# Kernel optimization log

Hardware: AMD Instinct MI355X
Metric: run time of the kernel (lower is better)

## Reference

```python
import jax, jax.numpy as jnp
import numpy as np

B, T, D = 4, 512, 512
NB, NH, PF, K = 2, 8, 2, 4
INNER = PF * D          # 1024
DH = INNER // NH        # 128
NC = 1000
EPS = 1e-5


def _ln(x, s, b):
    mu = x.mean(-1, keepdims=True)
    var = x.var(-1, keepdims=True)
    return (x - mu) / jnp.sqrt(var + EPS) * s + b


def _causal_conv(x, k, b):
    # x: [B,T,C], depthwise kernel k: [C,K]
    kk = k.shape[-1]
    xp = jnp.pad(x, ((0, 0), (kk - 1, 0), (0, 0)))
    t = x.shape[1]
    y = sum(xp[:, j:j + t, :] * k[:, j] for j in range(kk))
    return y + b


def _mlstm_scan(q, k, v, ip, fp):
    # q,k,v: [B,T,NH,DH]; ip,fp: [B,T,NH]
    b, t, nh, dh = q.shape
    C0 = jnp.zeros((b, nh, dh, dh), q.dtype)
    n0 = jnp.zeros((b, nh, dh), q.dtype)
    m0 = jnp.zeros((b, nh), q.dtype)

    def step(carry, xs):
        C, n, m = carry
        qt, kt, vt, ipt, fpt = xs
        fl = jax.nn.log_sigmoid(fpt)
        m_new = jnp.maximum(fl + m, ipt)
        i = jnp.exp(ipt - m_new)
        f = jnp.exp(fl + m - m_new)
        C = f[..., None, None] * C + i[..., None, None] * (vt[..., :, None] * kt[..., None, :])
        n = f[..., None] * n + i[..., None] * kt
        denom = jnp.maximum(jnp.abs(jnp.einsum('bhd,bhd->bh', n, qt)), 1.0)
        h = jnp.einsum('bhij,bhj->bhi', C, qt) / denom[..., None]
        return (C, n, m_new), h

    tm = lambda a: jnp.swapaxes(a, 0, 1)  # time-major
    _, h = jax.lax.scan(step, (C0, n0, m0), (tm(q), tm(k), tm(v), tm(ip), tm(fp)))
    return jnp.swapaxes(h, 0, 1)  # [B,T,NH,DH]


def _block(x, ln_s, ln_b, w_up, b_up, conv_k, conv_b, w_q, w_k, w_v,
           w_ig, b_ig, w_fg, b_fg, hn_s, w_down, b_down):
    b, t, d = x.shape
    xn = _ln(x, ln_s, ln_b)
    up = xn @ w_up + b_up                       # [B,T,2*INNER]
    xu, z = up[..., :INNER], up[..., INNER:]
    xc = jax.nn.silu(_causal_conv(xu, conv_k, conv_b))
    q = (xc @ w_q).reshape(b, t, NH, DH)
    k = (xc @ w_k).reshape(b, t, NH, DH) * (DH ** -0.5)
    v = (xu @ w_v).reshape(b, t, NH, DH)
    ip = xc @ w_ig + b_ig                       # [B,T,NH]
    fp = xc @ w_fg + b_fg
    h = _mlstm_scan(q, k, v, ip, fp)            # [B,T,NH,DH]
    mu = h.mean(-1, keepdims=True)
    var = h.var(-1, keepdims=True)
    h = (h - mu) / jnp.sqrt(var + EPS) * hn_s   # per-head norm, hn_s: [NH,DH]
    h = h.reshape(b, t, INNER) * jax.nn.silu(z)
    return x + h @ w_down + b_down


def setup_inputs() -> dict:
    key = jax.random.key(0)
    ks = jax.random.split(key, 24)
    g = lambda i, sh, sc: jax.random.normal(ks[i], sh, jnp.float32) * sc
    inp = {
        'x': g(0, (B, T, D), 1.0),
        'cls_token': g(1, (1, 1, D), 0.02),
        'ln_s': jnp.ones((NB, D)), 'ln_b': jnp.zeros((NB, D)),
        'w_up': g(2, (NB, D, 2 * INNER), D ** -0.5), 'b_up': jnp.zeros((NB, 2 * INNER)),
        'conv_k': g(3, (NB, INNER, K), 0.3), 'conv_b': jnp.zeros((NB, INNER)),
        'w_q': g(4, (NB, INNER, INNER), INNER ** -0.5),
        'w_k': g(5, (NB, INNER, INNER), INNER ** -0.5),
        'w_v': g(6, (NB, INNER, INNER), INNER ** -0.5),
        'w_ig': g(7, (NB, INNER, NH), INNER ** -0.5), 'b_ig': jnp.zeros((NB, NH)),
        'w_fg': g(8, (NB, INNER, NH), INNER ** -0.5),
        'b_fg': jnp.full((NB, NH), 3.0),
        'hn_s': jnp.ones((NB, NH, DH)),
        'w_down': g(9, (NB, INNER, D), INNER ** -0.5), 'b_down': jnp.zeros((NB, D)),
        'fc_ln_s': jnp.ones((D,)), 'fc_ln_b': jnp.zeros((D,)),
        'fc_w': g(10, (D, NC), D ** -0.5), 'fc_b': jnp.zeros((NC,)),
    }
    return inp


def reference(x, cls_token, ln_s, ln_b, w_up, b_up, conv_k, conv_b, w_q, w_k, w_v,
              w_ig, b_ig, w_fg, b_fg, hn_s, w_down, b_down,
              fc_ln_s, fc_ln_b, fc_w, fc_b):
    b = x.shape[0]
    # append class token at the last position ('last')
    h = jnp.concatenate([x, jnp.broadcast_to(cls_token, (b, 1, x.shape[-1]))], axis=1)
    for i in range(NB):
        h = _block(h, ln_s[i], ln_b[i], w_up[i], b_up[i], conv_k[i], conv_b[i],
                   w_q[i], w_k[i], w_v[i], w_ig[i], b_ig[i], w_fg[i], b_fg[i],
                   hn_s[i], w_down[i], b_down[i])
    cls = h[:, -1, :]
    y = jax.nn.relu(_ln(cls, fc_ln_s, fc_ln_b)) @ fc_w + fc_b
    return y
```

## Files before the change

kernel.cpp:

```cpp
#include <hip/hip_runtime.h>

#define EPSV 1e-5f
constexpr int Bsz = 4, T0 = 512, Dm = 512, TT = 513, NHh = 8, KK = 4;
constexpr int IN = 1024, DHd = 128, NCc = 1000;
constexpr int ROWS = Bsz * TT;
constexpr int MPAD = 2176;
constexpr int NCH = 9;

constexpr size_t WT_UP = 0;
constexpr size_t WT_Q  = WT_UP + 2048 * 512;
constexpr size_t WT_K  = WT_Q + 1024 * 1024;
constexpr size_t WT_V  = WT_K + 1024 * 1024;
constexpr size_t WT_DN = WT_V + 1024 * 1024;
constexpr size_t WT_STRIDE = WT_DN + 512 * 1024;

typedef __attribute__((ext_vector_type(8))) short bf16x8;
typedef __attribute__((ext_vector_type(4))) float f32x4;
typedef __attribute__((ext_vector_type(4))) unsigned short ushort4v;
typedef __attribute__((ext_vector_type(8))) unsigned short ushort8v;
typedef unsigned short u16;

__device__ __forceinline__ float siluf(float x) { return x / (1.f + __expf(-x)); }
__device__ __forceinline__ u16 f2bf(float f) {
    unsigned int u = __float_as_uint(f);
    u = (u + 0x7FFFu + ((u >> 16) & 1u)) >> 16;
    return (u16)u;
}
__device__ __forceinline__ float bfu(u16 u) {
    return __uint_as_float(((unsigned int)u) << 16);
}
__device__ __forceinline__ void gload16(const u16* g, u16* l) {
    __builtin_amdgcn_global_load_lds(
        (const __attribute__((address_space(1))) void*)g,
        (__attribute__((address_space(3))) void*)l, 16, 0, 0);
}

__global__ __launch_bounds__(256) void concat_kernel(const float* __restrict__ x,
                                                     const float* __restrict__ cls,
                                                     float* __restrict__ h) {
    int idx = blockIdx.x * 256 + threadIdx.x;
    if (idx >= Bsz * TT * Dm) return;
    int d = idx & (Dm - 1);
    int bt = idx >> 9;
    int t = bt % TT, b = bt / TT;
    h[idx] = (t < T0) ? x[((size_t)(b * T0 + t)) * Dm + d] : cls[d];
}

__global__ __launch_bounds__(256) void ln_kernel(const float* __restrict__ in,
                                                 const float* __restrict__ s,
                                                 const float* __restrict__ bb,
                                                 u16* __restrict__ out16) {
    int row = blockIdx.x, tid = threadIdx.x;
    const float* r = in + (size_t)row * Dm;
    __shared__ float s1[4], s2[4];
    float x0 = r[tid], x1 = r[tid + 256];
    float sum = x0 + x1, sq = x0 * x0 + x1 * x1;
#pragma unroll
    for (int o = 32; o > 0; o >>= 1) { sum += __shfl_xor(sum, o); sq += __shfl_xor(sq, o); }
    if ((tid & 63) == 0) { s1[tid >> 6] = sum; s2[tid >> 6] = sq; }
    __syncthreads();
    sum = s1[0] + s1[1] + s1[2] + s1[3];
    sq  = s2[0] + s2[1] + s2[2] + s2[3];
    float mu = sum / Dm, var = sq / Dm - mu * mu, inv = rsqrtf(var + EPSV);
    out16[(size_t)row * Dm + tid]       = f2bf((x0 - mu) * inv * s[tid] + bb[tid]);
    out16[(size_t)row * Dm + tid + 256] = f2bf((x1 - mu) * inv * s[tid + 256] + bb[tid + 256]);
}

__global__ __launch_bounds__(256) void w_transpose_kernel(const float* __restrict__ wup,
        const float* __restrict__ wq, const float* __restrict__ wk,
        const float* __restrict__ wv, const float* __restrict__ wdn,
        u16* __restrict__ wt) {
    int y = blockIdx.y;
    int blk = y / 5, sel = y - blk * 5;
    int Kd, N; const float* src; size_t doff;
    if (sel == 0)      { Kd = 512;  N = 2048; src = wup + (size_t)blk * 512 * 2048; doff = WT_UP; }
    else if (sel == 1) { Kd = 1024; N = 1024; src = wq  + (size_t)blk * 1024 * 1024; doff = WT_Q; }
    else if (sel == 2) { Kd = 1024; N = 1024; src = wk  + (size_t)blk * 1024 * 1024; doff = WT_K; }
    else if (sel == 3) { Kd = 1024; N = 1024; src = wv  + (size_t)blk * 1024 * 1024; doff = WT_V; }
    else               { Kd = 1024; N = 512;  src = wdn + (size_t)blk * 1024 * 512;  doff = WT_DN; }
    u16* dst = wt + (size_t)blk * WT_STRIDE + doff;
    int ntx = N >> 5;
    int ntiles = ntx * (Kd >> 5);
    int ti = blockIdx.x;
    if (ti >= ntiles) return;
    int tk = ti / ntx, tn = ti - tk * ntx;
    __shared__ u16 s[32][33];
    int tx = threadIdx.x & 31, ty = threadIdx.x >> 5;
#pragma unroll
    for (int i = 0; i < 4; i++) {
        int k = tk * 32 + ty + i * 8;
        s[ty + i * 8][tx] = f2bf(src[(size_t)k * N + tn * 32 + tx]);
    }
    __syncthreads();
#pragma unroll
    for (int i = 0; i < 4; i++) {
        int n = tn * 32 + ty + i * 8;
        dst[(size_t)n * Kd + tk * 32 + tx] = s[tx][ty + i * 8];
    }
}

template<int BM, int BN>
__device__ __forceinline__ void gemm_tile_body(const u16* __restrict__ A, int lda,
                                               const u16* __restrict__ Wt, int Kd,
                                               const float* __restrict__ bias,
                                               const float* __restrict__ resid, int ldr,
                                               float* __restrict__ Cout, int ldc,
                                               int M, float scale, int m0, int n0,
                                               u16 (*As)[BM][40], u16 (*Bs)[BN][40]) {
    constexpr int MT = BM / 32;
    constexpr int NT = BN / 32;
    constexpr int ANV = BM / 64;
    constexpr int BNV = BN / 64;
    int tid = threadIdx.x;
    int wave = tid >> 6, lane = tid & 63;
    int wm = (wave >> 1) * (BM / 2), wn = (wave & 1) * (BN / 2);
    int lrow = lane & 15, lquad = lane >> 4;

    f32x4 acc[MT][NT];
#pragma unroll
    for (int i = 0; i < MT; i++)
#pragma unroll
        for (int j = 0; j < NT; j++)
#pragma unroll
            for (int r = 0; r < 4; r++) acc[i][j][r] = 0.f;

    int am, ak, bn, bk;
    if (BM == 128) { am = tid >> 1; ak = (tid & 1) * 16; }
    else           { am = tid >> 2; ak = (tid & 3) * 8; }
    if (BN == 128) { bn = tid & 127; bk = (tid >> 7) * 16; }
    else           { bn = tid & 63;  bk = (tid >> 6) * 8; }
    int gm = m0 + am;
    const u16* arow = A + (size_t)(gm < M ? gm : 0) * lda + ak;
    bool avalid = gm < M;
    const u16* wrow = Wt + (size_t)(n0 + bn) * Kd + bk;

    ushort8v areg[ANV];
    ushort8v breg[BNV];

    auto load_tile = [&](int k0) {
        if (avalid) {
#pragma unroll
            for (int i = 0; i < ANV; i++) areg[i] = *(const ushort8v*)(arow + k0 + i * 8);
        } else {
#pragma unroll
            for (int i = 0; i < ANV; i++) areg[i] = (ushort8v){0,0,0,0,0,0,0,0};
        }
#pragma unroll
        for (int i = 0; i < BNV; i++) breg[i] = *(const ushort8v*)(wrow + k0 + i * 8);
    };
    auto store_tile = [&](int buf) {
#pragma unroll
        for (int i = 0; i < ANV; i++)
            *(ushort8v*)&As[buf][am][ak + i * 8] = areg[i];
#pragma unroll
        for (int i = 0; i < BNV; i++)
            *(ushort8v*)&Bs[buf][bn][bk + i * 8] = breg[i];
    };

    load_tile(0);
    store_tile(0);
    __syncthreads();

    int nk = Kd >> 5;
#pragma unroll 1
    for (int it = 0; it < nk; it++) {
        int cur = it & 1;
        bool more = (it + 1 < nk);
        if (more) load_tile((it + 1) << 5);
        bf16x8 afr[MT], bfr[NT];
#pragma unroll
        for (int mt = 0; mt < MT; mt++)
            afr[mt] = *(const bf16x8*)&As[cur][wm + mt * 16 + lrow][lquad * 8];
#pragma unroll
        for (int nt = 0; nt < NT; nt++)
            bfr[nt] = *(const bf16x8*)&Bs[cur][wn + nt * 16 + lrow][lquad * 8];
#pragma unroll
        for (int mt = 0; mt < MT; mt++)
#pragma unroll
            for (int nt = 0; nt < NT; nt++)
                acc[mt][nt] = __builtin_amdgcn_mfma_f32_16x16x32_bf16(
                    afr[mt], bfr[nt], acc[mt][nt], 0, 0, 0);
        if (more) store_tile(cur ^ 1);
        __syncthreads();
    }

#pragma unroll
    for (int mt = 0; mt < MT; mt++) {
#pragma unroll
        for (int r = 0; r < 4; r++) {
            int gmr = m0 + wm + mt * 16 + lquad * 4 + r;
            if (gmr >= M) continue;
#pragma unroll
            for (int nt = 0; nt < NT; nt++) {
                int gn = n0 + wn + nt * 16 + lrow;
                float v = acc[mt][nt][r] * scale;
                if (bias) v += bias[gn];
                if (resid) v += resid[(size_t)gmr * ldr + gn];
                Cout[(size_t)gmr * ldc + gn] = v;
            }
        }
    }
}

template<int BM, int BN>
__global__ __launch_bounds__(256, 2) void gemm_mfma_kernel(const u16* __restrict__ A, int lda,
                                                           const u16* __restrict__ Wt, int Kd,
                                                           const float* __restrict__ bias,
                                                           const float* __restrict__ resid, int ldr,
                                                           float* __restrict__ Cout, int ldc,
                                                           int M, float scale) {
    __shared__ __align__(16) u16 As[2][BM][40];
    __shared__ __align__(16) u16 Bs[2][BN][40];
    gemm_tile_body<BM, BN>(A, lda, Wt, Kd, bias, resid, ldr, Cout, ldc, M, scale,
                           blockIdx.y * BM, blockIdx.x * BN, As, Bs);
}

__device__ __forceinline__ void gemm128_body(const u16* __restrict__ A, int lda,
                                             const u16* __restrict__ Wt, int Kd,
                                             const float* __restrict__ bias,
                                             float* __restrict__ Cout, int ldc,
                                             int M, float scale, int m0, int n0,
                                             u16* As, u16* Bs) {
    int tid = threadIdx.x;
    int wave = tid >> 6, lane = tid & 63;
    int lrow = lane & 15, lquad = lane >> 4;
    int wm = (wave >> 1) * 64, wn = (wave & 1) * 64;

    const u16* ag0 = A + (size_t)(m0 + wave * 16 + (lane >> 2)) * lda + (lane & 3) * 8;
    const u16* ag1 = ag0 + (size_t)64 * lda;
    const u16* bg0 = Wt + (size_t)(n0 + wave * 16 + (lane >> 2)) * Kd + (lane & 3) * 8;
    const u16* bg1 = bg0 + (size_t)64 * Kd;
    u16* la0 = As + wave * 512;
    u16* la1 = As + 2048 + wave * 512;
    u16* lb0 = Bs + wave * 512;
    u16* lb1 = Bs + 2048 + wave * 512;

    f32x4 acc[4][4];
#pragma unroll
    for (int i = 0; i < 4; i++)
#pragma unroll
        for (int j = 0; j < 4; j++)
#pragma unroll
            for (int r = 0; r < 4; r++) acc[i][j][r] = 0.f;

    int nk = Kd >> 5;
#pragma unroll 1
    for (int it = 0; it < nk; it++) {
        int k0 = it << 5;
        gload16(ag0 + k0, la0);
        gload16(ag1 + k0, la1);
        gload16(bg0 + k0, lb0);
        gload16(bg1 + k0, lb1);
        __syncthreads();
        bf16x8 afr[4], bfr[4];
#pragma unroll
        for (int mt = 0; mt < 4; mt++)
            afr[mt] = *(const bf16x8*)&As[(wm + mt * 16 + lrow) * 32 + lquad * 8];
#pragma unroll
        for (int nt = 0; nt < 4; nt++)
            bfr[nt] = *(const bf16x8*)&Bs[(wn + nt * 16 + lrow) * 32 + lquad * 8];
#pragma unroll
        for (int mt = 0; mt < 4; mt++)
#pragma unroll
            for (int nt = 0; nt < 4; nt++)
                acc[mt][nt] = __builtin_amdgcn_mfma_f32_16x16x32_bf16(
                    afr[mt], bfr[nt], acc[mt][nt], 0, 0, 0);
        __syncthreads();
    }

#pragma unroll
    for (int mt = 0; mt < 4; mt++) {
#pragma unroll
        for (int r = 0; r < 4; r++) {
            int gmr = m0 + wm + mt * 16 + lquad * 4 + r;
            if (gmr >= M) continue;
#pragma unroll
            for (int nt = 0; nt < 4; nt++) {
                int gn = n0 + wn + nt * 16 + lrow;
                float v = acc[mt][nt][r] * scale;
                if (bias) v += bias[gn];
                Cout[(size_t)gmr * ldc + gn] = v;
            }
        }
    }
}

__global__ __launch_bounds__(256, 2) void up_gl_kernel(const u16* __restrict__ A,
        const u16* __restrict__ Wt, const float* __restrict__ bias, float* __restrict__ C) {
    __shared__ __align__(16) u16 As[128 * 32];
    __shared__ __align__(16) u16 Bs[128 * 32];
    gemm128_body(A, Dm, Wt, Dm, bias, C, 2 * IN, ROWS, 1.f,
                 blockIdx.y * 128, blockIdx.x * 128, As, Bs);
}

__global__ __launch_bounds__(256, 2) void qkv_gl_kernel(const u16* __restrict__ xc16,
                                                        const u16* __restrict__ xu16,
                                                        const u16* __restrict__ wtblk,
                                                        float* __restrict__ fq,
                                                        float* __restrict__ fk,
                                                        float* __restrict__ fv,
                                                        float kscale) {
    __shared__ __align__(16) u16 As[128 * 32];
    __shared__ __align__(16) u16 Bs[128 * 32];
    int sel = blockIdx.x >> 3, nx = blockIdx.x & 7;
    const u16* A = (sel == 2) ? xu16 : xc16;
    const u16* Wt = wtblk + ((sel == 0) ? WT_Q : (sel == 1) ? WT_K : WT_V);
    float* C = (sel == 0) ? fq : (sel == 1) ? fk : fv;
    float scale = (sel == 1) ? kscale : 1.f;
    gemm128_body(A, IN, Wt, IN, nullptr, C, IN, ROWS, scale,
                 blockIdx.y * 128, nx * 128, As, Bs);
}

__global__ __launch_bounds__(256) void convgates_kernel(const float* __restrict__ up,
        const float* __restrict__ ck, const float* __restrict__ cb,
        const float* __restrict__ wt, const float* __restrict__ big,
        const float* __restrict__ bfg,
        u16* __restrict__ xc16, u16* __restrict__ xu16,
        float* __restrict__ ip, float* __restrict__ fp) {
    int row = blockIdx.x, tid = threadIdx.x;
    int b = row / TT, t = row - b * TT;
    __shared__ float sx[IN];
    int c0 = tid * 4;
    float4 cur = *(const float4*)(up + (size_t)row * (2 * IN) + c0);
    float a0 = cb[c0 + 0] + cur.x * ck[(c0 + 0) * KK + 3];
    float a1 = cb[c0 + 1] + cur.y * ck[(c0 + 1) * KK + 3];
    float a2 = cb[c0 + 2] + cur.z * ck[(c0 + 2) * KK + 3];
    float a3 = cb[c0 + 3] + cur.w * ck[(c0 + 3) * KK + 3];
#pragma unroll
    for (int j = 0; j < KK - 1; j++) {
        int tt2 = t - (KK - 1) + j;
        if (tt2 >= 0) {
            float4 pv = *(const float4*)(up + ((size_t)(b * TT + tt2)) * (2 * IN) + c0);
            a0 += pv.x * ck[(c0 + 0) * KK + j];
            a1 += pv.y * ck[(c0 + 1) * KK + j];
            a2 += pv.z * ck[(c0 + 2) * KK + j];
            a3 += pv.w * ck[(c0 + 3) * KK + j];
        }
    }
    float s0 = siluf(a0), s1v = siluf(a1), s2v = siluf(a2), s3v = siluf(a3);
    *(float4*)&sx[c0] = make_float4(s0, s1v, s2v, s3v);
    ushort4v xc4 = {f2bf(s0), f2bf(s1v), f2bf(s2v), f2bf(s3v)};
    *(ushort4v*)&xc16[(size_t)row * IN + c0] = xc4;
    ushort4v xu4 = {f2bf(cur.x), f2bf(cur.y), f2bf(cur.z), f2bf(cur.w)};
    *(ushort4v*)&xu16[(size_t)row * IN + c0] = xu4;
    __syncthreads();

    int g = tid >> 4, l = tid & 15;
    const float* wrow = wt + g * IN;
    float acc = 0.f;
#pragma unroll
    for (int j = 0; j < 16; j++) {
        int k = j * 64 + l * 4;
        float4 w4 = *(const float4*)(wrow + k);
        float4 x4 = *(const float4*)&sx[k];
        acc += w4.x * x4.x + w4.y * x4.y + w4.z * x4.z + w4.w * x4.w;
    }
#pragma unroll
    for (int o = 8; o > 0; o >>= 1) acc += __shfl_down(acc, o, 16);
    if (l == 0) {
        if (g < 8) ip[(size_t)row * NHh + g] = acc + big[g];
        else       fp[(size_t)row * NHh + (g - 8)] = acc + bfg[g - 8];
    }
}

__global__ __launch_bounds__(64) void gate_scan_kernel(const float* __restrict__ ip,
        const float* __restrict__ fp, float* __restrict__ gG, float* __restrict__ gM,
        float* __restrict__ gMb, float* __restrict__ gDec) {
    constexpr int PER = 9;
    int chain = blockIdx.x;
    int b = chain >> 3, h = chain & 7;
    int lane = threadIdx.x;
    int tbase = lane * PER;
    float lcs[PER];
    float gi[PER];
    float csum = 0.f;
#pragma unroll
    for (int i = 0; i < PER; i++) {
        int t = tbase + i;
        float fpv = 0.f, ipv = 0.f;
        if (t < TT) {
            size_t gidx = (size_t)(b * TT + t) * NHh + h;
            fpv = fp[gidx]; ipv = ip[gidx];
        }
        float flv = (fpv >= 0.f) ? -log1pf(__expf(-fpv)) : (fpv - log1pf(__expf(fpv)));
        if (t >= TT) flv = 0.f;
        csum += flv;
        lcs[i] = csum;
        gi[i] = ipv;
    }
    float ps = csum;
#pragma unroll
    for (int o = 1; o < 64; o <<= 1) {
        float v = __shfl_up(ps, o);
        if (lane >= o) ps += v;
    }
    float Fexcl = ps - csum;
    float G[PER];
    float cmax = -1e30f;
#pragma unroll
    for (int i = 0; i < PER; i++) {
        int t = tbase + i;
        G[i] = (t < TT) ? (gi[i] - (Fexcl + lcs[i])) : -1e30f;
        cmax = fmaxf(cmax, G[i]);
        lcs[i] = cmax;
    }
    float pm = cmax;
#pragma unroll
    for (int o = 1; o < 64; o <<= 1) {
        float v = __shfl_up(pm, o);
        if (lane >= o) pm = fmaxf(pm, v);
    }
    float Me = __shfl_up(pm, 1);
    if (lane == 0) Me = -1e30f;
    __shared__ float sMb[NCH];
#pragma unroll
    for (int i = 0; i < PER; i++) {
        int t = tbase + i;
        if (t < TT) {
            float Mt = fmaxf(0.f, fmaxf(Me, lcs[i]));
            gG[chain * TT + t] = G[i];
            gM[chain * TT + t] = Mt;
            if (((t & 63) == 63) || t == TT - 1) sMb[t >> 6] = Mt;
        }
    }
    __syncthreads();
    if (lane < NCH) {
        float Mb = sMb[lane];
        float Mbp = (lane == 0) ? 0.f : sMb[lane - 1];
        gMb[chain * NCH + lane] = Mb;
        gDec[chain * NCH + lane] = __expf(Mbp - Mb);
    }
}

__global__ __launch_bounds__(256, 2) void chunk_state_kernel(const float* __restrict__ kk,
        const float* __restrict__ vv, const float* __restrict__ gG,
        const float* __restrict__ gMb, float* __restrict__ P, float* __restrict__ nP) {
    int c = blockIdx.x, chain = blockIdx.y;
    int b = chain >> 3, h = chain & 7;
    int t0 = c * 64;
    int nvalid = min(64, TT - t0);
    __shared__ __align__(16) u16 sWv[128][72];
    __shared__ __align__(16) u16 sKt[128][72];
    __shared__ float sw[64];
    int tid = threadIdx.x;
    if (tid < 64) {
        float Mb = gMb[chain * NCH + c];
        sw[tid] = (tid < nvalid) ? __expf(gG[chain * TT + t0 + tid] - Mb) : 0.f;
    }
    __syncthreads();

    {
        int j = tid >> 2, d0 = (tid & 3) * 32;
        bool val = j < nvalid;
        float wj = sw[j];
        size_t gb = ((size_t)(b * TT + t0 + j)) * IN + h * DHd + d0;
#pragma unroll
        for (int i = 0; i < 8; i++) {
            float4 k4 = val ? *(const float4*)(kk + gb + i * 4) : make_float4(0.f, 0.f, 0.f, 0.f);
            float4 v4 = val ? *(const float4*)(vv + gb + i * 4) : make_float4(0.f, 0.f, 0.f, 0.f);
            int dd = d0 + i * 4;
            int jc = j ^ (((dd >> 5) & 3) << 4);
            sKt[dd + 0][jc] = f2bf(k4.x);
            sKt[dd + 1][jc] = f2bf(k4.y);
            sKt[dd + 2][jc] = f2bf(k4.z);
            sKt[dd + 3][jc] = f2bf(k4.w);
            sWv[dd + 0][jc] = f2bf(v4.x * wj);
            sWv[dd + 1][jc] = f2bf(v4.y * wj);
            sWv[dd + 2][jc] = f2bf(v4.z * wj);
            sWv[dd + 3][jc] = f2bf(v4.w * wj);
        }
    }
    __syncthreads();

    int wave = tid >> 6, lane = tid & 63;
    int lrow = lane & 15, lquad = lane >> 4;
    int wm = (wave >> 1) * 64, wn = (wave & 1) * 64;
    f32x4 acc[4][4];
#pragma unroll
    for (int mt = 0; mt < 4; mt++)
#pragma unroll
        for (int nt = 0; nt < 4; nt++)
#pragma unroll
            for (int r = 0; r < 4; r++) acc[mt][nt][r] = 0.f;

#pragma unroll
    for (int ks = 0; ks < 2; ks++) {
        bf16x8 af[4], bfr[4];
#pragma unroll
        for (int mt = 0; mt < 4; mt++) {
            int r = wm + mt * 16 + lrow;
            int g = (ks * 4 + lquad) ^ (((r >> 5) & 3) << 1);
            af[mt] = *(const bf16x8*)&sWv[r][g * 8];
        }
#pragma unroll
        for (int nt = 0; nt < 4; nt++) {
            int r = wn + nt * 16 + lrow;
            int g = (ks * 4 + lquad) ^ (((r >> 5) & 3) << 1);
            bfr[nt] = *(const bf16x8*)&sKt[r][g * 8];
        }
#pragma unroll
        for (int mt = 0; mt < 4; mt++)
#pragma unroll
            for (int nt = 0; nt < 4; nt++)
                acc[mt][nt] = __builtin_amdgcn_mfma_f32_16x16x32_bf16(
                    af[mt], bfr[nt], acc[mt][nt], 0, 0, 0);
    }

    float* Pbase = P + (((size_t)(c * 32 + chain)) << 14);
#pragma unroll
    for (int mt = 0; mt < 4; mt++)
#pragma unroll
        for (int r = 0; r < 4; r++) {
            int e = wm + mt * 16 + lquad * 4 + r;
#pragma unroll
            for (int nt = 0; nt < 4; nt++) {
                int d = wn + nt * 16 + lrow;
                Pbase[(size_t)e * 128 + d] = acc[mt][nt][r];
            }
        }

    {
        int d = tid >> 1, jh = (tid & 1) * 32;
        int swz = ((d >> 5) & 3) << 4;
        float an = 0.f;
#pragma unroll
        for (int j = 0; j < 32; j++) {
            int jj = jh + j;
            an += sw[jj] * bfu(sKt[d][jj ^ swz]);
        }
        an += __shfl_xor(an, 1);
        if ((tid & 1) == 0) nP[(size_t)(c * 32 + chain) * 128 + d] = an;
    }
}

__global__ __launch_bounds__(256) void chunk_combine_kernel(const float* __restrict__ P,
        u16* __restrict__ CB, float* __restrict__ nP, const float* __restrict__ gDec) {
    int chain = blockIdx.x >> 6;
    int seg = blockIdx.x & 63;
    int idx = seg * 256 + threadIdx.x;
    float run = 0.f;
    for (int c = 0; c < NCH; c++) {
        size_t a = (((size_t)(c * 32 + chain)) << 14) + idx;
        float tmp = P[a];
        CB[a] = f2bf(run);
        run = run * gDec[chain * NCH + c] + tmp;
    }
    if (seg == 0 && threadIdx.x < 128) {
        int d = threadIdx.x;
        float rn = 0.f;
        for (int c = 0; c < NCH; c++) {
            size_t a = (size_t)(c * 32 + chain) * 128 + d;
            float tmp = nP[a];
            nP[a] = rn;
            rn = rn * gDec[chain * NCH + c] + tmp;
        }
    }
}

__global__ __launch_bounds__(512, 2) void chunk_out_kernel(const float* __restrict__ qq,
        const float* __restrict__ kk, const float* __restrict__ vv,
        const float* __restrict__ gG, const float* __restrict__ gM,
        const float* __restrict__ gMb, const u16* __restrict__ CB,
        const float* __restrict__ nP, const float* __restrict__ hn,
        const float* __restrict__ up, u16* __restrict__ out16) {
    int c = blockIdx.x, chain = blockIdx.y;
    int b = chain >> 3, h = chain & 7;
    int t0 = c * 64;
    int nvalid = min(64, TT - t0);
    __shared__ __align__(16) u16 smem[30720];
    __shared__ float sG[64], sM[64], sWr[64], sInv[64], sNb[128], sRS[2][64];
    u16* sQ  = smem;
    u16* sCB = smem + 8704;
    u16* sK  = smem + 8704;
    u16* sVt = smem;
    u16* sD  = smem + 26112;
    float* hv = (float*)smem;
    int tid = threadIdx.x;
    int wave = tid >> 6, lane = tid & 63;
    int lrow = lane & 15, lquad = lane >> 4;
    int mq = wave >> 1, nh = wave & 1;

    float Mbprev = (c > 0) ? gMb[chain * NCH + c - 1] : 0.f;
    if (tid < 64) {
        bool val = tid < nvalid;
        sG[tid] = val ? gG[chain * TT + t0 + tid] : -1e30f;
        float Mv = val ? gM[chain * TT + t0 + tid] : 1e30f;
        sM[tid] = Mv;
        sWr[tid] = val ? __expf(Mbprev - Mv) : 0.f;
    }
    if (tid >= 128 && tid < 256) sNb[tid - 128] = nP[(size_t)(c * 32 + chain) * 128 + (tid - 128)];

    {
        int lr = tid >> 3, c0 = (tid & 7) * 16;
        bool val = lr < nvalid;
        size_t gb = ((size_t)(b * TT + t0 + lr)) * IN + h * DHd + c0;
#pragma unroll
        for (int i = 0; i < 4; i++) {
            float4 q4 = val ? *(const float4*)(qq + gb + i * 4) : make_float4(0.f,0.f,0.f,0.f);
            ushort4v tq = {f2bf(q4.x), f2bf(q4.y), f2bf(q4.z), f2bf(q4.w)};
            *(ushort4v*)&sQ[lr * 136 + c0 + i * 4] = tq;
        }
    }
    {
        const u16* CBbase = CB + (((size_t)(c * 32 + chain)) << 14);
        int e = tid >> 2, d0 = (tid & 3) * 32;
#pragma unroll
        for (int i = 0; i < 4; i++)
            *(ushort8v*)&sCB[e * 136 + d0 + i * 8] =
                *(const ushort8v*)(CBbase + (size_t)e * 128 + d0 + i * 8);
    }
    __syncthreads();

    f32x4 acc[4];
#pragma unroll
    for (int tt = 0; tt < 4; tt++)
#pragma unroll
        for (int r = 0; r < 4; r++) acc[tt][r] = 0.f;
#pragma unroll 1
    for (int ks = 0; ks < 4; ks++) {
        bf16x8 af = *(const bf16x8*)&sQ[(mq * 16 + lrow) * 136 + ks * 32 + lquad * 8];
#pragma unroll
        for (int tt = 0; tt < 4; tt++) {
            bf16x8 bf = *(const bf16x8*)&sCB[(nh * 64 + tt * 16 + lrow) * 136 + ks * 32 + lquad * 8];
            acc[tt] = __builtin_amdgcn_mfma_f32_16x16x32_bf16(af, bf, acc[tt], 0, 0, 0);
        }
    }
#pragma unroll
    for (int tt = 0; tt < 4; tt++)
#pragma unroll
        for (int r = 0; r < 4; r++) acc[tt][r] *= sWr[mq * 16 + lquad * 4 + r];
    __syncthreads();

    {
        int lr = tid >> 3, c0 = (tid & 7) * 16;
        bool val = lr < nvalid;
        size_t gb = ((size_t)(b * TT + t0 + lr)) * IN + h * DHd + c0;
#pragma unroll
        for (int i = 0; i < 4; i++) {
            float4 k4 = val ? *(const float4*)(kk + gb + i * 4) : make_float4(0.f,0.f,0.f,0.f);
            ushort4v tk = {f2bf(k4.x), f2bf(k4.y), f2bf(k4.z), f2bf(k4.w)};
            *(ushort4v*)&sK[lr * 136 + c0 + i * 4] = tk;
        }
    }
    __syncthreads();

    {
        f32x4 accS[2];
#pragma unroll
        for (int tt = 0; tt < 2; tt++)
#pragma unroll
            for (int r = 0; r < 4; r++) accS[tt][r] = 0.f;
#pragma unroll 1
        for (int ks = 0; ks < 4; ks++) {
            bf16x8 af = *(const bf16x8*)&sQ[(mq * 16 + lrow) * 136 + ks * 32 + lquad * 8];
#pragma unroll
            for (int tt = 0; tt < 2; tt++) {
                bf16x8 bf = *(const bf16x8*)&sK[((nh * 2 + tt) * 16 + lrow) * 136 + ks * 32 + lquad * 8];
                accS[tt] = __builtin_amdgcn_mfma_f32_16x16x32_bf16(af, bf, accS[tt], 0, 0, 0);
            }
        }
        float rsum[4] = {0.f, 0.f, 0.f, 0.f};
#pragma unroll
        for (int tt = 0; tt < 2; tt++) {
            int j = (nh * 2 + tt) * 16 + lrow;
            float Gj = sG[j];
#pragma unroll
            for (int r = 0; r < 4; r++) {
                int t = mq * 16 + lquad * 4 + r;
                float w = (j <= t) ? __expf(Gj - sM[t]) : 0.f;
                float wD = accS[tt][r] * w;
                rsum[r] += wD;
                sD[t * 72 + j] = f2bf(wD);
            }
        }
#pragma unroll
        for (int r = 0; r < 4; r++) {
#pragma unroll
            for (int msk = 1; msk < 16; msk <<= 1) rsum[r] += __shfl_xor(rsum[r], msk);
        }
        if (lrow == 0) {
#pragma unroll
            for (int r = 0; r < 4; r++) sRS[nh][mq * 16 + lquad * 4 + r] = rsum[r];
        }
    }
    __syncthreads();

    if (tid < 64) {
        float qn = 0.f;
#pragma unroll 1
        for (int d4 = 0; d4 < 32; d4++) {
            ushort4v q4 = *(const ushort4v*)&sQ[tid * 136 + d4 * 4];
            float4 nb = *(const float4*)&sNb[d4 * 4];
            qn += bfu(q4.x) * nb.x + bfu(q4.y) * nb.y + bfu(q4.z) * nb.z + bfu(q4.w) * nb.w;
        }
        float den = sRS[0][tid] + sRS[1][tid] + sWr[tid] * qn;
        sInv[tid] = 1.f / fmaxf(fabsf(den), 1.f);
    }
    __syncthreads();

    {
        int e = tid & 127, tg = (tid >> 7) * 16;
#pragma unroll 1
        for (int i = 0; i < 16; i++) {
            int t = tg + i;
            float v = (t < nvalid) ? vv[((size_t)(b * TT + t0 + t)) * IN + h * DHd + e] : 0.f;
            sVt[e * 72 + t] = f2bf(v);
        }
    }
    __syncthreads();

#pragma unroll 1
    for (int ks = 0; ks < 2; ks++) {
        bf16x8 af = *(const bf16x8*)&sD[(mq * 16 + lrow) * 72 + ks * 32 + lquad * 8];
#pragma unroll
        for (int tt = 0; tt < 4; tt++) {
            bf16x8 bf = *(const bf16x8*)&sVt[(nh * 64 + tt * 16 + lrow) * 72 + ks * 32 + lquad * 8];
            acc[tt] = __builtin_amdgcn_mfma_f32_16x16x32_bf16(af, bf, acc[tt], 0, 0, 0);
        }
    }

    __syncthreads();
#pragma unroll
    for (int tt = 0; tt < 4; tt++) {
#pragma unroll
        for (int r = 0; r < 4; r++) {
            int t = mq * 16 + lquad * 4 + r;
            int e = nh * 64 + tt * 16 + lrow;
            hv[t * 132 + e] = acc[tt][r] * sInv[t];
        }
    }
    __syncthreads();
    {
        int t = tid >> 3, s = tid & 7;
        float vals[16];
        float sum = 0.f, sq = 0.f;
#pragma unroll
        for (int i = 0; i < 16; i++) {
            float v = hv[t * 132 + s * 16 + i];
            vals[i] = v; sum += v; sq += v * v;
        }
#pragma unroll
        for (int m = 1; m < 8; m <<= 1) { sum += __shfl_xor(sum, m); sq += __shfl_xor(sq, m); }
        float mu = sum / DHd, var = sq / DHd - mu * mu, inv2 = rsqrtf(var + EPSV);
        if (t < nvalid) {
            size_t bt = (size_t)(b * TT + t0 + t);
            const float* zp = up + bt * (2 * IN) + IN + h * DHd + s * 16;
            u16* op = out16 + bt * IN + h * DHd + s * 16;
#pragma unroll
            for (int i = 0; i < 16; i++) {
                float hnv = hn[h * DHd + s * 16 + i];
                op[i] = f2bf((vals[i] - mu) * inv2 * hnv * siluf(zp[i]));
            }
        }
    }
}

__global__ __launch_bounds__(256) void fc_kernel(const float* __restrict__ hbuf,
                                                 const float* __restrict__ fcls,
                                                 const float* __restrict__ fclb,
                                                 const float* __restrict__ fw,
                                                 const float* __restrict__ fb,
                                                 float* __restrict__ out) {
    __shared__ float svc[Bsz][Dm];
    __shared__ float sred[4][256];
    int tid = threadIdx.x;
    int j0 = blockIdx.x * 64;
    {
        int r = tid >> 6, lane = tid & 63;
        const float* hrow = hbuf + ((size_t)r * TT + TT - 1) * Dm;
        float v[8];
        float sum = 0.f, sq = 0.f;
#pragma unroll
        for (int k = 0; k < 8; k++) {
            v[k] = hrow[lane + k * 64];
            sum += v[k]; sq += v[k] * v[k];
        }
#pragma unroll
        for (int o = 32; o > 0; o >>= 1) { sum += __shfl_xor(sum, o); sq += __shfl_xor(sq, o); }
        float mu = sum / Dm, var = sq / Dm - mu * mu, inv = rsqrtf(var + EPSV);
#pragma unroll
        for (int k = 0; k < 8; k++) {
            int e = lane + k * 64;
            svc[r][e] = fmaxf((v[k] - mu) * inv * fcls[e] + fclb[e], 0.f);
        }
    }
    __syncthreads();
    int j = j0 + (tid & 63);
    int chunk = tid >> 6;
    int kbase = chunk * 128;
    float a0 = 0.f, a1 = 0.f, a2 = 0.f, a3 = 0.f;
    if (j < NCc) {
        const float* fwp = fw + (size_t)kbase * NCc + j;
#pragma unroll 4
        for (int kk = 0; kk < 128; kk++) {
            float w = fwp[(size_t)kk * NCc];
            a0 += svc[0][kbase + kk] * w;
            a1 += svc[1][kbase + kk] * w;
            a2 += svc[2][kbase + kk] * w;
            a3 += svc[3][kbase + kk] * w;
        }
    }
    int jl = tid & 63;
    sred[chunk][jl * 4 + 0] = a0;
    sred[chunk][jl * 4 + 1] = a1;
    sred[chunk][jl * 4 + 2] = a2;
    sred[chunk][jl * 4 + 3] = a3;
    __syncthreads();
    if (tid < 64) {
        int jj = j0 + tid;
        if (jj < NCc) {
            float bias = fb[jj];
#pragma unroll
            for (int b = 0; b < Bsz; b++) {
                float v = sred[0][tid * 4 + b] + sred[1][tid * 4 + b]
                        + sred[2][tid * 4 + b] + sred[3][tid * 4 + b];
                out[b * NCc + jj] = v + bias;
            }
        }
    }
}

__global__ __launch_bounds__(256) void gate_w_transpose(const float* __restrict__ wig,
                                                        const float* __restrict__ wfg,
                                                        float* __restrict__ wt) {
    int idx = blockIdx.x * 256 + threadIdx.x;
    int k = idx & 1023;
    int g = (idx >> 10) & 15;
    int blk = idx >> 14;
    const float* w = (g < 8) ? (wig + (size_t)blk * IN * NHh) : (wfg + (size_t)blk * IN * NHh);
    wt[idx] = w[k * NHh + (g & 7)];
}

extern "C" void kernel_launch(void* const* d_in, const int* in_sizes, int n_in,
                              void* d_out, int out_size, void* d_ws, size_t ws_size,
                              hipStream_t stream) {
    const float* x      = (const float*)d_in[0];
    const float* cls    = (const float*)d_in[1];
    const float* ln_s   = (const float*)d_in[2];
    const float* ln_b   = (const float*)d_in[3];
    const float* w_up   = (const float*)d_in[4];
    const float* b_up   = (const float*)d_in[5];
    const float* conv_k = (const float*)d_in[6];
    const float* conv_b = (const float*)d_in[7];
    const float* w_q    = (const float*)d_in[8];
    const float* w_k    = (const float*)d_in[9];
    const float* w_v    = (const float*)d_in[10];
    const float* w_ig   = (const float*)d_in[11];
    const float* b_ig   = (const float*)d_in[12];
    const float* w_fg   = (const float*)d_in[13];
    const float* b_fg   = (const float*)d_in[14];
    const float* hn_s   = (const float*)d_in[15];
    const float* w_down = (const float*)d_in[16];
    const float* b_down = (const float*)d_in[17];
    const float* fcls   = (const float*)d_in[18];
    const float* fclb   = (const float*)d_in[19];
    const float* fc_w   = (const float*)d_in[20];
    const float* fc_b   = (const float*)d_in[21];
    float* out = (float*)d_out;

    float* ws = (float*)d_ws;
    size_t off = 0;
    float* f_h  = ws + off; off += (size_t)ROWS * Dm;
    float* f_up = ws + off; off += (size_t)ROWS * 2 * IN;
    float* f_q  = ws + off; off += (size_t)ROWS * IN;
    float* f_k  = ws + off; off += (size_t)ROWS * IN;
    float* f_v  = ws + off; off += (size_t)ROWS * IN;
    float* f_ip = ws + off; off += (size_t)ROWS * NHh;
    float* f_fp = ws + off; off += (size_t)ROWS * NHh;
    float* g_G  = ws + off; off += 32 * TT;
    float* g_M  = ws + off; off += 32 * TT;
    float* g_Mb = ws + off; off += 32 * NCH;
    float* g_De = ws + off; off += 32 * NCH;
    float* g_P  = ws + off; off += (size_t)NCH * 32 * DHd * DHd;
    float* g_nP = ws + off; off += (size_t)NCH * 32 * DHd;
    float* g_wt = ws + off; off += 2 * 16 * IN;
    u16* g_CB  = (u16*)(ws + off); off += ((size_t)NCH * 32 * DHd * DHd + 1) / 2;
    u16* g_Wt  = (u16*)(ws + off); off += (2 * WT_STRIDE + 1) / 2;
    u16* f_xn16 = (u16*)(ws + off); off += ((size_t)MPAD * Dm) / 2;
    u16* f_xc16 = (u16*)(ws + off); off += ((size_t)MPAD * IN) / 2;
    u16* f_xu16 = (u16*)(ws + off); off += ((size_t)MPAD * IN) / 2;
    u16* f_xg16 = (u16*)(ws + off); off += ((size_t)ROWS * IN + 1) / 2;

    const float kscale = 0.08838834764831845f;
    const int MB = (ROWS + 127) / 128;
    const int MB64 = (ROWS + 63) / 64;

    concat_kernel<<<(ROWS * Dm + 255) / 256, 256, 0, stream>>>(x, cls, f_h);
    gate_w_transpose<<<(2 * 16 * IN + 255) / 256, 256, 0, stream>>>(w_ig, w_fg, g_wt);
    w_transpose_kernel<<<dim3(1024, 10), 256, 0, stream>>>(w_up, w_q, w_k, w_v, w_down, g_Wt);

    for (int blk = 0; blk < 2; blk++) {
        const float* p_ln_s = ln_s + blk * Dm;
        const float* p_ln_b = ln_b + blk * Dm;
        const float* p_bup  = b_up + (size_t)blk * 2 * IN;
        const float* p_ck   = conv_k + (size_t)blk * IN * KK;
        const float* p_cb   = conv_b + (size_t)blk * IN;
        const float* p_big  = b_ig + (size_t)blk * NHh;
        const float* p_bfg  = b_fg + (size_t)blk * NHh;
        const float* p_hns  = hn_s + (size_t)blk * NHh * DHd;
        const float* p_bd   = b_down + (size_t)blk * Dm;
        const u16*   p_wt   = g_Wt + (size_t)blk * WT_STRIDE;

        ln_kernel<<<ROWS, 256, 0, stream>>>(f_h, p_ln_s, p_ln_b, f_xn16);

        up_gl_kernel<<<dim3(2 * IN / 128, MB), 256, 0, stream>>>(
            f_xn16, p_wt + WT_UP, p_bup, f_up);

        convgates_kernel<<<ROWS, 256, 0, stream>>>(
            f_up, p_ck, p_cb, g_wt + blk * 16 * IN, p_big, p_bfg,
            f_xc16, f_xu16, f_ip, f_fp);

        qkv_gl_kernel<<<dim3(24, MB), 256, 0, stream>>>(
            f_xc16, f_xu16, p_wt, f_q, f_k, f_v, kscale);

        gate_scan_kernel<<<32, 64, 0, stream>>>(f_ip, f_fp, g_G, g_M, g_Mb, g_De);
        chunk_state_kernel<<<dim3(NCH, 32), 256, 0, stream>>>(f_k, f_v, g_G, g_Mb, g_P, g_nP);
        chunk_combine_kernel<<<32 * 64, 256, 0, stream>>>(g_P, g_CB, g_nP, g_De);
        chunk_out_kernel<<<dim3(NCH, 32), 512, 0, stream>>>(f_q, f_k, f_v, g_G, g_M, g_Mb,
                                                            g_CB, g_nP, p_hns, f_up, f_xg16);

        gemm_mfma_kernel<64, 64><<<dim3(Dm / 64, MB64), 256, 0, stream>>>(
            f_xg16, IN, p_wt + WT_DN, IN, p_bd, f_h, Dm, f_h, Dm, ROWS, 1.f);
    }

    fc_kernel<<<(NCc + 63) / 64, 256, 0, stream>>>(f_h, fcls, fclb, fc_w, fc_b, out);
}
```

Measured before the change: 435.4 us.

## Store q/k/v as bf16 and double-buffer LDS in 128-tile GEMM

```diff
diff --git a/kernel.cpp b/kernel.cpp
--- a/kernel.cpp
+++ b/kernel.cpp
@@ -1,7 +1,8 @@
 #include <hip/hip_runtime.h>
 
 #define EPSV 1e-5f
-constexpr int Bsz = 4, T0 = 512, Dm = 512, TT = 513, NHh = 8, KK = 4;
+constexpr int Bsz = 4, T0 = 512, Dm = 512, NHh = 8, KK = 4;
+constexpr int TT = 513;
 constexpr int IN = 1024, DHd = 128, NCc = 1000;
 constexpr int ROWS = Bsz * TT;
 constexpr int MPAD = 2176;
@@ -215,10 +216,11 @@
                            blockIdx.y * BM, blockIdx.x * BN, As, Bs);
 }
 
+template<bool OUT16>
 __device__ __forceinline__ void gemm128_body(const u16* __restrict__ A, int lda,
                                              const u16* __restrict__ Wt, int Kd,
                                              const float* __restrict__ bias,
-                                             float* __restrict__ Cout, int ldc,
+                                             void* __restrict__ Cout, int ldc,
                                              int M, float scale, int m0, int n0,
                                              u16* As, u16* Bs) {
     int tid = threadIdx.x;
@@ -230,10 +232,15 @@
     const u16* ag1 = ag0 + (size_t)64 * lda;
     const u16* bg0 = Wt + (size_t)(n0 + wave * 16 + (lane >> 2)) * Kd + (lane & 3) * 8;
     const u16* bg1 = bg0 + (size_t)64 * Kd;
-    u16* la0 = As + wave * 512;
-    u16* la1 = As + 2048 + wave * 512;
-    u16* lb0 = Bs + wave * 512;
-    u16* lb1 = Bs + 2048 + wave * 512;
+
+    auto stage = [&](int buf, int k0) {
+        u16* a = As + buf * 4096 + wave * 512;
+        u16* bb = Bs + buf * 4096 + wave * 512;
+        gload16(ag0 + k0, a);
+        gload16(ag1 + k0, a + 2048);
+        gload16(bg0 + k0, bb);
+        gload16(bg1 + k0, bb + 2048);
+    };
 
     f32x4 acc[4][4];
 #pragma unroll
@@ -244,21 +251,21 @@
             for (int r = 0; r < 4; r++) acc[i][j][r] = 0.f;
 
     int nk = Kd >> 5;
+    stage(0, 0);
+    __syncthreads();
 #pragma unroll 1
     for (int it = 0; it < nk; it++) {
-        int k0 = it << 5;
-        gload16(ag0 + k0, la0);
-        gload16(ag1 + k0, la1);
-        gload16(bg0 + k0, lb0);
-        gload16(bg1 + k0, lb1);
-        __syncthreads();
+        int cur = it & 1;
+        if (it + 1 < nk) stage(cur ^ 1, (it + 1) << 5);
+        const u16* Ac = As + cur * 4096;
+        const u16* Bc = Bs + cur * 4096;
         bf16x8 afr[4], bfr[4];
 #pragma unroll
         for (int mt = 0; mt < 4; mt++)
-            afr[mt] = *(const bf16x8*)&As[(wm + mt * 16 + lrow) * 32 + lquad * 8];
+            afr[mt] = *(const bf16x8*)&Ac[(wm + mt * 16 + lrow) * 32 + lquad * 8];
 #pragma unroll
         for (int nt = 0; nt < 4; nt++)
-            bfr[nt] = *(const bf16x8*)&Bs[(wn + nt * 16 + lrow) * 32 + lquad * 8];
+            bfr[nt] = *(const bf16x8*)&Bc[(wn + nt * 16 + lrow) * 32 + lquad * 8];
 #pragma unroll
         for (int mt = 0; mt < 4; mt++)
 #pragma unroll
@@ -279,7 +286,8 @@
                 int gn = n0 + wn + nt * 16 + lrow;
                 float v = acc[mt][nt][r] * scale;
                 if (bias) v += bias[gn];
-                Cout[(size_t)gmr * ldc + gn] = v;
+                if (OUT16) ((u16*)Cout)[(size_t)gmr * ldc + gn] = f2bf(v);
+                else       ((float*)Cout)[(size_t)gmr * ldc + gn] = v;
             }
         }
     }
@@ -287,28 +295,28 @@
 
 __global__ __launch_bounds__(256, 2) void up_gl_kernel(const u16* __restrict__ A,
         const u16* __restrict__ Wt, const float* __restrict__ bias, float* __restrict__ C) {
-    __shared__ __align__(16) u16 As[128 * 32];
-    __shared__ __align__(16) u16 Bs[128 * 32];
-    gemm128_body(A, Dm, Wt, Dm, bias, C, 2 * IN, ROWS, 1.f,
-                 blockIdx.y * 128, blockIdx.x * 128, As, Bs);
+    __shared__ __align__(16) u16 As[2 * 4096];
+    __shared__ __align__(16) u16 Bs[2 * 4096];
+    gemm128_body<false>(A, Dm, Wt, Dm, bias, C, 2 * IN, ROWS, 1.f,
+                        blockIdx.y * 128, blockIdx.x * 128, As, Bs);
 }
 
 __global__ __launch_bounds__(256, 2) void qkv_gl_kernel(const u16* __restrict__ xc16,
                                                         const u16* __restrict__ xu16,
                                                         const u16* __restrict__ wtblk,
-                                                        float* __restrict__ fq,
-                                                        float* __restrict__ fk,
-                                                        float* __restrict__ fv,
+                                                        u16* __restrict__ fq,
+                                                        u16* __restrict__ fk,
+                                                        u16* __restrict__ fv,
                                                         float kscale) {
-    __shared__ __align__(16) u16 As[128 * 32];
-    __shared__ __align__(16) u16 Bs[128 * 32];
+    __shared__ __align__(16) u16 As[2 * 4096];
+    __shared__ __align__(16) u16 Bs[2 * 4096];
     int sel = blockIdx.x >> 3, nx = blockIdx.x & 7;
     const u16* A = (sel == 2) ? xu16 : xc16;
     const u16* Wt = wtblk + ((sel == 0) ? WT_Q : (sel == 1) ? WT_K : WT_V);
-    float* C = (sel == 0) ? fq : (sel == 1) ? fk : fv;
+    u16* C = (sel == 0) ? fq : (sel == 1) ? fk : fv;
     float scale = (sel == 1) ? kscale : 1.f;
-    gemm128_body(A, IN, Wt, IN, nullptr, C, IN, ROWS, scale,
-                 blockIdx.y * 128, nx * 128, As, Bs);
+    gemm128_body<true>(A, IN, Wt, IN, nullptr, C, IN, ROWS, scale,
+                       blockIdx.y * 128, nx * 128, As, Bs);
 }
 
 __global__ __launch_bounds__(256) void convgates_kernel(const float* __restrict__ up,
@@ -432,8 +440,8 @@
     }
 }
 
-__global__ __launch_bounds__(256, 2) void chunk_state_kernel(const float* __restrict__ kk,
-        const float* __restrict__ vv, const float* __restrict__ gG,
+__global__ __launch_bounds__(256, 2) void chunk_state_kernel(const u16* __restrict__ kk,
+        const u16* __restrict__ vv, const float* __restrict__ gG,
         const float* __restrict__ gMb, float* __restrict__ P, float* __restrict__ nP) {
     int c = blockIdx.x, chain = blockIdx.y;
     int b = chain >> 3, h = chain & 7;
@@ -454,20 +462,18 @@
         bool val = j < nvalid;
         float wj = sw[j];
         size_t gb = ((size_t)(b * TT + t0 + j)) * IN + h * DHd + d0;
-#pragma unroll
-        for (int i = 0; i < 8; i++) {
-            float4 k4 = val ? *(const float4*)(kk + gb + i * 4) : make_float4(0.f, 0.f, 0.f, 0.f);
-            float4 v4 = val ? *(const float4*)(vv + gb + i * 4) : make_float4(0.f, 0.f, 0.f, 0.f);
-            int dd = d0 + i * 4;
-            int jc = j ^ (((dd >> 5) & 3) << 4);
-            sKt[dd + 0][jc] = f2bf(k4.x);
-            sKt[dd + 1][jc] = f2bf(k4.y);
-            sKt[dd + 2][jc] = f2bf(k4.z);
-            sKt[dd + 3][jc] = f2bf(k4.w);
-            sWv[dd + 0][jc] = f2bf(v4.x * wj);
-            sWv[dd + 1][jc] = f2bf(v4.y * wj);
-            sWv[dd + 2][jc] = f2bf(v4.z * wj);
-            sWv[dd + 3][jc] = f2bf(v4.w * wj);
+        ushort8v z8 = {0,0,0,0,0,0,0,0};
+#pragma unroll
+        for (int i = 0; i < 4; i++) {
+            ushort8v k8 = val ? *(const ushort8v*)(kk + gb + i * 8) : z8;
+            ushort8v v8 = val ? *(const ushort8v*)(vv + gb + i * 8) : z8;
+#pragma unroll
+            for (int e = 0; e < 8; e++) {
+                int dd = d0 + i * 8 + e;
+                int jc = j ^ (((dd >> 5) & 3) << 4);
+                sKt[dd][jc] = k8[e];
+                sWv[dd][jc] = f2bf(bfu(v8[e]) * wj);
+            }
         }
     }
     __syncthreads();
@@ -557,8 +563,8 @@
     }
 }
 
-__global__ __launch_bounds__(512, 2) void chunk_out_kernel(const float* __restrict__ qq,
-        const float* __restrict__ kk, const float* __restrict__ vv,
+__global__ __launch_bounds__(512, 2) void chunk_out_kernel(const u16* __restrict__ qq,
+        const u16* __restrict__ kk, const u16* __restrict__ vv,
         const float* __restrict__ gG, const float* __restrict__ gM,
         const float* __restrict__ gMb, const u16* __restrict__ CB,
         const float* __restrict__ nP, const float* __restrict__ hn,
@@ -590,16 +596,15 @@
     }
     if (tid >= 128 && tid < 256) sNb[tid - 128] = nP[(size_t)(c * 32 + chain) * 128 + (tid - 128)];
 
+    ushort8v z8 = {0,0,0,0,0,0,0,0};
     {
         int lr = tid >> 3, c0 = (tid & 7) * 16;
         bool val = lr < nvalid;
         size_t gb = ((size_t)(b * TT + t0 + lr)) * IN + h * DHd + c0;
 #pragma unroll
-        for (int i = 0; i < 4; i++) {
-            float4 q4 = val ? *(const float4*)(qq + gb + i * 4) : make_float4(0.f,0.f,0.f,0.f);
-            ushort4v tq = {f2bf(q4.x), f2bf(q4.y), f2bf(q4.z), f2bf(q4.w)};
-            *(ushort4v*)&sQ[lr * 136 + c0 + i * 4] = tq;
-        }
+        for (int i = 0; i < 2; i++)
+            *(ushort8v*)&sQ[lr * 136 + c0 + i * 8] =
+                val ? *(const ushort8v*)(qq + gb + i * 8) : z8;
     }
     {
         const u16* CBbase = CB + (((size_t)(c * 32 + chain)) << 14);
@@ -636,11 +641,9 @@
         bool val = lr < nvalid;
         size_t gb = ((size_t)(b * TT + t0 + lr)) * IN + h * DHd + c0;
 #pragma unroll
-        for (int i = 0; i < 4; i++) {
-            float4 k4 = val ? *(const float4*)(kk + gb + i * 4) : make_float4(0.f,0.f,0.f,0.f);
-            ushort4v tk = {f2bf(k4.x), f2bf(k4.y), f2bf(k4.z), f2bf(k4.w)};
-            *(ushort4v*)&sK[lr * 136 + c0 + i * 4] = tk;
-        }
+        for (int i = 0; i < 2; i++)
+            *(ushort8v*)&sK[lr * 136 + c0 + i * 8] =
+                val ? *(const ushort8v*)(kk + gb + i * 8) : z8;
     }
     __syncthreads();
 
@@ -703,8 +706,8 @@
 #pragma unroll 1
         for (int i = 0; i < 16; i++) {
             int t = tg + i;
-            float v = (t < nvalid) ? vv[((size_t)(b * TT + t0 + t)) * IN + h * DHd + e] : 0.f;
-            sVt[e * 72 + t] = f2bf(v);
+            sVt[e * 72 + t] = (t < nvalid) ? vv[((size_t)(b * TT + t0 + t)) * IN + h * DHd + e]
+                                           : (u16)0;
         }
     }
     __syncthreads();
@@ -862,9 +865,6 @@
     size_t off = 0;
     float* f_h  = ws + off; off += (size_t)ROWS * Dm;
     float* f_up = ws + off; off += (size_t)ROWS * 2 * IN;
-    float* f_q  = ws + off; off += (size_t)ROWS * IN;
-    float* f_k  = ws + off; off += (size_t)ROWS * IN;
-    float* f_v  = ws + off; off += (size_t)ROWS * IN;
     float* f_ip = ws + off; off += (size_t)ROWS * NHh;
     float* f_fp = ws + off; off += (size_t)ROWS * NHh;
     float* g_G  = ws + off; off += 32 * TT;
@@ -880,6 +880,9 @@
     u16* f_xc16 = (u16*)(ws + off); off += ((size_t)MPAD * IN) / 2;
     u16* f_xu16 = (u16*)(ws + off); off += ((size_t)MPAD * IN) / 2;
     u16* f_xg16 = (u16*)(ws + off); off += ((size_t)ROWS * IN + 1) / 2;
+    u16* f_q16  = (u16*)(ws + off); off += ((size_t)ROWS * IN + 1) / 2;
+    u16* f_k16  = (u16*)(ws + off); off += ((size_t)ROWS * IN + 1) / 2;
+    u16* f_v16  = (u16*)(ws + off); off += ((size_t)ROWS * IN + 1) / 2;
 
     const float kscale = 0.08838834764831845f;
     const int MB = (ROWS + 127) / 128;
@@ -911,12 +914,12 @@
             f_xc16, f_xu16, f_ip, f_fp);
 
         qkv_gl_kernel<<<dim3(24, MB), 256, 0, stream>>>(
-            f_xc16, f_xu16, p_wt, f_q, f_k, f_v, kscale);
+            f_xc16, f_xu16, p_wt, f_q16, f_k16, f_v16, kscale);
 
         gate_scan_kernel<<<32, 64, 0, stream>>>(f_ip, f_fp, g_G, g_M, g_Mb, g_De);
-        chunk_state_kernel<<<dim3(NCH, 32), 256, 0, stream>>>(f_k, f_v, g_G, g_Mb, g_P, g_nP);
+        chunk_state_kernel<<<dim3(NCH, 32), 256, 0, stream>>>(f_k16, f_v16, g_G, g_Mb, g_P, g_nP);
         chunk_combine_kernel<<<32 * 64, 256, 0, stream>>>(g_P, g_CB, g_nP, g_De);
-        chunk_out_kernel<<<dim3(NCH, 32), 512, 0, stream>>>(f_q, f_k, f_v, g_G, g_M, g_Mb,
+        chunk_out_kernel<<<dim3(NCH, 32), 512, 0, stream>>>(f_q16, f_k16, f_v16, g_G, g_M, g_Mb,
                                                             g_CB, g_nP, p_hns, f_up, f_xg16);
 
         gemm_mfma_kernel<64, 64><<<dim3(Dm / 64, MB64), 256, 0, stream>>>(
```

Result: faster. 419.1 us (-3.7%).
